# Performance work log

Measured on AMD Instinct MI355X. Metric: run time of the kernel, lower is better.

Reference implementation:

```python
import jax, jax.numpy as jnp
import numpy as np

HIDDEN = 1024
HEADS = 16
HEAD_DIM = HIDDEN // HEADS
B, S = 2, 2048


def setup_inputs() -> dict:
    key = jax.random.key(0)
    k1, k2, k3 = jax.random.split(key, 3)
    x = jax.random.normal(k1, (B, S, HIDDEN), dtype=jnp.float32)
    qkv_w = jax.random.normal(k2, (3 * HIDDEN, HIDDEN), dtype=jnp.float32) * (HIDDEN ** -0.5)
    out_w = jax.random.normal(k3, (HIDDEN, HIDDEN), dtype=jnp.float32) * (HIDDEN ** -0.5)
    return {"x": x, "qkv_w": qkv_w, "out_w": out_w}


def reference(x, qkv_w, out_w):
    b, s, d = x.shape
    scale = HEAD_DIM ** -0.5
    # qkv projection (Linear without bias: x @ W^T)
    qkv = x @ qkv_w.T                                   # [b, s, 3d]
    qkv = qkv.reshape(b, s, 3, HEADS, HEAD_DIM)
    qkv = jnp.transpose(qkv, (2, 0, 3, 1, 4))           # [3, b, h, s, hd]
    q, k, v = qkv[0] * scale, qkv[1], qkv[2]
    # causal attention (blocked torch loop == full causal softmax attention)
    scores = jnp.einsum('bhqd,bhkd->bhqk', q, k)        # [b, h, s, s]
    causal = jnp.tril(jnp.ones((s, s), dtype=bool))
    scores = jnp.where(causal[None, None], scores, -jnp.inf)
    weights = jax.nn.softmax(scores, axis=-1)
    attn = jnp.einsum('bhqk,bhkd->bhqd', weights, v)    # [b, h, s, hd]
    attn = jnp.transpose(attn, (0, 2, 1, 3)).reshape(b, s, d)
    return attn @ out_w.T
```

## Files before the change

### kernel.cpp

```cpp
#include <hip/hip_runtime.h>
#include <hip/hip_bf16.h>
#include <math.h>

#define HIDDEN 1024
#define HEADS 16
#define HDIM 64
#define BATCH 2
#define SEQ 2048
#define BHN (BATCH*HEADS)
#define MTOT (BATCH*SEQ)

typedef __attribute__((ext_vector_type(8))) short short8;
typedef __attribute__((ext_vector_type(4))) short short4v;
typedef __attribute__((ext_vector_type(4))) float floatx4;

#define GL2LDS(gsrc, ldst) __builtin_amdgcn_global_load_lds( \
    (const __attribute__((address_space(1))) void*)(gsrc), \
    (__attribute__((address_space(3))) void*)(ldst), 16, 0, 0)

__device__ __forceinline__ short f2bf(float f) {
  union { float f; unsigned u; } v; v.f = f;
  unsigned u = v.u;
  unsigned r = (u + 0x7fffu + ((u >> 16) & 1u)) >> 16;
  return (short)r;
}

__global__ __launch_bounds__(256) void cvt3_f32_bf16(
    const float* __restrict__ a, const float* __restrict__ b, const float* __restrict__ c,
    short* __restrict__ oa, short* __restrict__ ob, short* __restrict__ oc) {
  int i = blockIdx.x * 256 + threadIdx.x;
  const float* src; short* dst; int j;
  if (i < 1048576)      { src = a; dst = oa; j = i; }
  else if (i < 1835008) { src = b; dst = ob; j = i - 1048576; }
  else                  { src = c; dst = oc; j = i - 1835008; }
  float4 f = reinterpret_cast<const float4*>(src)[j];
  short4 o;
  o.x = f2bf(f.x); o.y = f2bf(f.y); o.z = f2bf(f.z); o.w = f2bf(f.w);
  reinterpret_cast<short4*>(dst)[j] = o;
}

template<int EPI, int BN>
__global__ __launch_bounds__(256) void gemm_bt(
    const short* __restrict__ A, const short* __restrict__ B,
    int M, int N, int K,
    float* __restrict__ outF,
    short* __restrict__ outQ, short* __restrict__ outK, short* __restrict__ outV)
{
  constexpr int WN = BN / 2;
  constexpr int NI = BN / 32;
  constexpr int BRD = BN / 32;
  __shared__ __align__(16) short As[128*64];
  __shared__ __align__(16) short Bs[BN*64];
  const int tid = threadIdx.x;
  const int wv = tid >> 6;
  const int lane = tid & 63;
  const int l15 = lane & 15;
  const int quad = lane >> 4;
  const int swl = l15 & 7;
  const int wm = wv >> 1, wn = wv & 1;

  const int nwg = gridDim.x * gridDim.y;
  const int cpx = nwg >> 3;
  int wg = (int)blockIdx.y * gridDim.x + blockIdx.x;
  wg = (wg & 7) * cpx + (wg >> 3);
  const int bx = wg % gridDim.x, by = wg / gridDim.x;
  const int row0 = by * 128, col0 = bx * BN;

  const int nsteps = K >> 6;

  const short* aSrc[4];
#pragma unroll
  for (int rd = 0; rd < 4; ++rd) {
    int chunk = rd * 256 + tid;
    int r = chunk >> 3, c = ((chunk & 7) ^ (r & 7)) << 3;
    aSrc[rd] = A + (long)(row0 + r) * K + c;
  }
  const short* bSrc[BRD];
#pragma unroll
  for (int rd = 0; rd < BRD; ++rd) {
    int chunk = rd * 256 + tid;
    int r = chunk >> 3, c = ((chunk & 7) ^ (r & 7)) << 3;
    bSrc[rd] = B + (long)(col0 + r) * K + c;
  }

  floatx4 acc[4][NI];
#pragma unroll
  for (int i = 0; i < 4; i++)
#pragma unroll
    for (int j = 0; j < NI; j++) acc[i][j] = (floatx4){0.f, 0.f, 0.f, 0.f};

  for (int t = 0; t < nsteps; ++t) {
#pragma unroll
    for (int rd = 0; rd < 4; ++rd) {
      GL2LDS(aSrc[rd], As + (rd * 256 + wv * 64) * 8);
      aSrc[rd] += 64;
    }
#pragma unroll
    for (int rd = 0; rd < BRD; ++rd) {
      GL2LDS(bSrc[rd], Bs + (rd * 256 + wv * 64) * 8);
      bSrc[rd] += 64;
    }
    __syncthreads();

    short8 af[4][2], bfr[NI][2];
#pragma unroll
    for (int mi = 0; mi < 4; mi++) {
      const short* ap = As + (wm * 64 + mi * 16 + l15) * 64;
#pragma unroll
      for (int kk = 0; kk < 2; kk++)
        af[mi][kk] = *(const short8*)(ap + (((kk * 4 + quad) ^ swl) << 3));
    }
#pragma unroll
    for (int ni = 0; ni < NI; ni++) {
      const short* bp = Bs + (wn * WN + ni * 16 + l15) * 64;
#pragma unroll
      for (int kk = 0; kk < 2; kk++)
        bfr[ni][kk] = *(const short8*)(bp + (((kk * 4 + quad) ^ swl) << 3));
    }
    __builtin_amdgcn_s_setprio(1);
#pragma unroll
    for (int mi = 0; mi < 4; mi++)
#pragma unroll
      for (int ni = 0; ni < NI; ni++)
#pragma unroll
        for (int kk = 0; kk < 2; kk++)
          acc[mi][ni] = __builtin_amdgcn_mfma_f32_16x16x32_bf16(af[mi][kk], bfr[ni][kk], acc[mi][ni], 0, 0, 0);
    __builtin_amdgcn_s_setprio(0);
    __syncthreads();
  }

  if (EPI == 2) {
#pragma unroll
    for (int mi = 0; mi < 4; mi++) {
      int rr = row0 + wm * 64 + mi * 16 + quad * 4;
#pragma unroll
      for (int ni = 0; ni < NI; ni++) {
        int cc = col0 + wn * WN + ni * 16 + l15;
#pragma unroll
        for (int r = 0; r < 4; r++)
          outF[(long)(rr + r) * N + cc] = acc[mi][ni][r];
      }
    }
  } else {
#pragma unroll
    for (int mi = 0; mi < 4; mi++) {
      int rowg = row0 + wm * 64 + mi * 16 + quad * 4;
#pragma unroll
      for (int ni = 0; ni < NI; ni++) {
        int j = col0 + wn * WN + ni * 16 + l15;
        int t = j >> 10;
        int rem = j & 1023;
        int h = rem >> 6, d = rem & 63;
#pragma unroll
        for (int r = 0; r < 4; r++) {
          int i = rowg + r;
          int b = i >> 11, s = i & 2047;
          int bh = b * HEADS + h;
          float v = acc[mi][ni][r];
          if (t == 0)      outQ[(bh * SEQ + s) * HDIM + d] = f2bf(v * 0.18033688011112042f);
          else if (t == 1) outK[(bh * SEQ + s) * HDIM + d] = f2bf(v);
          else             outV[(bh * HDIM + d) * SEQ + s] = f2bf(v);
        }
      }
    }
  }
}

__global__ __launch_bounds__(256, 4) void flash_attn(
    const short* __restrict__ qg, const short* __restrict__ kg,
    const short* __restrict__ vT, short* __restrict__ attn)
{
  __shared__ __align__(16) short Ks[2][64 * 64];
  __shared__ __align__(16) short Vs[2][64 * 64];

  const int tid = threadIdx.x;
  const int wv = tid >> 6, lane = tid & 63;
  const int l15 = lane & 15, quad = lane >> 4;
  const int bh = blockIdx.x;
  const int yl = (int)blockIdx.y;
  const int sgrp = yl >> 3, y0 = yl & 7;
  const int yp = ((sgrp >> 1) << 4) + ((sgrp & 1) ? (15 - y0) : y0);
  const int rt = 31 - yp;
  const int qh = wv >> 1;
  const int kh = wv & 1;
  const int m0 = rt * 64 + qh * 32;
  const int swl = l15 & 7;

  const short* kPtr[2];
  const short* vPtr[2];
  int ldsOff[2];
#pragma unroll
  for (int i = 0; i < 2; ++i) {
    int slot = i * 256 + tid;
    int r = slot >> 3;
    int c = ((slot & 7) ^ (r & 7)) << 3;
    kPtr[i] = kg + (bh * SEQ + r) * HDIM + c;
    vPtr[i] = vT + (bh * HDIM + r) * SEQ + c;
    ldsOff[i] = (i * 256 + wv * 64) * 8;
  }
#define STAGE_KV(KsB, VsB)                              \
  do {                                                  \
    _Pragma("unroll")                                   \
    for (int i = 0; i < 2; ++i) {                       \
      GL2LDS(kPtr[i], (KsB) + ldsOff[i]);               \
      GL2LDS(vPtr[i], (VsB) + ldsOff[i]);               \
      kPtr[i] += 64 * HDIM;                             \
      vPtr[i] += 64;                                    \
    }                                                   \
  } while (0)

  short8 aq[2][2];
#pragma unroll
  for (int g = 0; g < 2; g++) {
    const short* qp = qg + (long)(bh * SEQ + m0 + g * 16 + l15) * HDIM + quad * 8;
    aq[g][0] = *(const short8*)qp;
    aq[g][1] = *(const short8*)(qp + 32);
  }

  const short ONE = (short)0x3F80;
  const short4v ones4 = {ONE, ONE, ONE, ONE};

  floatx4 o[2][4], lsum[2];
#pragma unroll
  for (int g = 0; g < 2; g++) {
    lsum[g] = (floatx4){0.f, 0.f, 0.f, 0.f};
#pragma unroll
    for (int nt = 0; nt < 4; nt++) o[g][nt] = (floatx4){0.f, 0.f, 0.f, 0.f};
  }

  const int ntiles = rt + 1;
  STAGE_KV(Ks[0], Vs[0]);

  for (int kt = 0; kt < ntiles; ++kt) {
    __syncthreads();
    const int buf = kt & 1;
    if (kt + 1 < ntiles)
      STAGE_KV(Ks[buf ^ 1], Vs[buf ^ 1]);

    const short* KsB = Ks[buf];
    const short* VsB = Vs[buf];

    floatx4 sc[2][2];
#pragma unroll
    for (int g = 0; g < 2; g++)
#pragma unroll
      for (int sub = 0; sub < 2; sub++) sc[g][sub] = (floatx4){0.f, 0.f, 0.f, 0.f};
    __builtin_amdgcn_s_setprio(1);
#pragma unroll
    for (int sub = 0; sub < 2; sub++) {
      const short* kp = KsB + (kh * 32 + sub * 16 + l15) * 64;
      short8 kf0 = *(const short8*)(kp + ((quad ^ swl) << 3));
      short8 kf1 = *(const short8*)(kp + (((4 + quad) ^ swl) << 3));
#pragma unroll
      for (int g = 0; g < 2; g++) {
        sc[g][sub] = __builtin_amdgcn_mfma_f32_16x16x32_bf16(kf0, aq[g][0], sc[g][sub], 0, 0, 0);
        sc[g][sub] = __builtin_amdgcn_mfma_f32_16x16x32_bf16(kf1, aq[g][1], sc[g][sub], 0, 0, 0);
      }
    }
    __builtin_amdgcn_s_setprio(0);

    short4v pa[2][2];
#pragma unroll
    for (int g = 0; g < 2; g++) {
      const int qrow = m0 + g * 16 + l15;
#pragma unroll
      for (int sub = 0; sub < 2; sub++) {
        const int kbase = kt * 64 + kh * 32 + sub * 16;
        const bool full = (kbase + 15) <= (m0 + g * 16);
        unsigned u[4];
#pragma unroll
        for (int r = 0; r < 4; r++) {
          float pe = __builtin_amdgcn_exp2f(sc[g][sub][r]);
          if (!full) {
            const int kpos = kbase + quad * 4 + r;
            pe = (kpos <= qrow) ? pe : 0.f;
          }
          u[r] = __builtin_bit_cast(unsigned, pe);
        }
        uint2 w;
        w.x = __builtin_amdgcn_perm(u[1], u[0], 0x07060302);
        w.y = __builtin_amdgcn_perm(u[3], u[2], 0x07060302);
        pa[g][sub] = __builtin_bit_cast(short4v, w);
      }
    }

    __builtin_amdgcn_s_setprio(1);
#pragma unroll
    for (int sub = 0; sub < 2; sub++) {
      short4v bv[4];
#pragma unroll
      for (int nt = 0; nt < 4; nt++) {
        const int ch = (kh * 4 + sub * 2 + (quad >> 1)) ^ swl;
        bv[nt] = *(const short4v*)(VsB + (nt * 16 + l15) * 64 + (ch << 3) + ((quad & 1) << 2));
      }
#pragma unroll
      for (int g = 0; g < 2; g++) {
        lsum[g] = __builtin_amdgcn_mfma_f32_16x16x16bf16_1k(pa[g][sub], ones4, lsum[g], 0, 0, 0);
#pragma unroll
        for (int nt = 0; nt < 4; nt++)
          o[g][nt] = __builtin_amdgcn_mfma_f32_16x16x16bf16_1k(pa[g][sub], bv[nt], o[g][nt], 0, 0, 0);
      }
    }
    __builtin_amdgcn_s_setprio(0);
  }
#undef STAGE_KV

  __syncthreads();
  float* redO = (float*)&Ks[0][0];
  float* redL = (float*)&Vs[0][0];
  const int thr = qh * 64 + lane;
  if (kh == 1) {
#pragma unroll
    for (int g = 0; g < 2; g++) {
#pragma unroll
      for (int nt = 0; nt < 4; nt++)
#pragma unroll
        for (int r = 0; r < 4; r++)
          redO[(g * 16 + nt * 4 + r) * 128 + thr] = o[g][nt][r];
#pragma unroll
      for (int r = 0; r < 4; r++) redL[(g * 4 + r) * 128 + thr] = lsum[g][r];
    }
  }
  __syncthreads();
  if (kh == 0) {
    const int b = bh >> 4, h = bh & 15;
#pragma unroll
    for (int g = 0; g < 2; g++) {
      floatx4 lt = lsum[g];
#pragma unroll
      for (int r = 0; r < 4; r++) lt[r] += redL[(g * 4 + r) * 128 + thr];
#pragma unroll
      for (int r = 0; r < 4; r++) {
        const float inv = 1.0f / lt[r];
        const int srow = m0 + g * 16 + quad * 4 + r;
#pragma unroll
        for (int nt = 0; nt < 4; nt++) {
          float val = o[g][nt][r] + redO[(g * 16 + nt * 4 + r) * 128 + thr];
          attn[(long)(b * SEQ + srow) * HIDDEN + h * HDIM + nt * 16 + l15] = f2bf(val * inv);
        }
      }
    }
  }
}

extern "C" void kernel_launch(void* const* d_in, const int* in_sizes, int n_in,
                              void* d_out, int out_size, void* d_ws, size_t ws_size,
                              hipStream_t stream) {
  const float* x     = (const float*)d_in[0];
  const float* qkv_w = (const float*)d_in[1];
  const float* out_w = (const float*)d_in[2];
  float* out = (float*)d_out;

  short* xb   = (short*)d_ws;
  short* wqb  = xb  + MTOT * HIDDEN;
  short* wob  = wqb + 3 * HIDDEN * HIDDEN;
  short* qB   = wob + HIDDEN * HIDDEN;
  short* kB   = qB  + BHN * SEQ * HDIM;
  short* vTB  = kB  + BHN * SEQ * HDIM;
  short* attn = vTB + BHN * SEQ * HDIM;

  cvt3_f32_bf16<<<dim3(8192), dim3(256), 0, stream>>>(x, qkv_w, out_w, xb, wqb, wob);

  gemm_bt<1, 128><<<dim3(3 * HIDDEN / 128, MTOT / 128), dim3(256), 0, stream>>>(
      xb, wqb, MTOT, 3 * HIDDEN, HIDDEN, nullptr, qB, kB, vTB);

  flash_attn<<<dim3(BHN, SEQ / 64), dim3(256), 0, stream>>>(qB, kB, vTB, attn);

  gemm_bt<2, 64><<<dim3(HIDDEN / 64, MTOT / 128), dim3(256), 0, stream>>>(
      attn, wob, MTOT, HIDDEN, HIDDEN, out, nullptr, nullptr, nullptr);
}
```

Measured before the change: 171.4 us.

## Load K/V fragments directly from global memory, dropping LDS double-buffering

Removes the LDS staging of K and V tiles and the per-tile barrier. Each wave now loads its own K and V MFMA fragments straight from global memory into registers, and LDS is kept only for the final cross-wave reduction. This is meant to remove the barrier and LDS round-trip costs. In exchange, the two q-half waves sharing a kh slice read the same K/V data from global/L2 redundantly, and without prefetch the global load latency sits directly on the critical path.

After: 223.5 us. 30.5% more time.

```diff
diff --git a/kernel.cpp b/kernel.cpp
--- a/kernel.cpp
+++ b/kernel.cpp
@@ -170,8 +170,8 @@
     const short* __restrict__ qg, const short* __restrict__ kg,
     const short* __restrict__ vT, short* __restrict__ attn)
 {
-  __shared__ __align__(16) short Ks[2][64 * 64];
-  __shared__ __align__(16) short Vs[2][64 * 64];
+  __shared__ float redO[32 * 128];
+  __shared__ float redL[8 * 128];
 
   const int tid = threadIdx.x;
   const int wv = tid >> 6, lane = tid & 63;
@@ -184,30 +184,6 @@
   const int qh = wv >> 1;
   const int kh = wv & 1;
   const int m0 = rt * 64 + qh * 32;
-  const int swl = l15 & 7;
-
-  const short* kPtr[2];
-  const short* vPtr[2];
-  int ldsOff[2];
-#pragma unroll
-  for (int i = 0; i < 2; ++i) {
-    int slot = i * 256 + tid;
-    int r = slot >> 3;
-    int c = ((slot & 7) ^ (r & 7)) << 3;
-    kPtr[i] = kg + (bh * SEQ + r) * HDIM + c;
-    vPtr[i] = vT + (bh * HDIM + r) * SEQ + c;
-    ldsOff[i] = (i * 256 + wv * 64) * 8;
-  }
-#define STAGE_KV(KsB, VsB)                              \
-  do {                                                  \
-    _Pragma("unroll")                                   \
-    for (int i = 0; i < 2; ++i) {                       \
-      GL2LDS(kPtr[i], (KsB) + ldsOff[i]);               \
-      GL2LDS(vPtr[i], (VsB) + ldsOff[i]);               \
-      kPtr[i] += 64 * HDIM;                             \
-      vPtr[i] += 64;                                    \
-    }                                                   \
-  } while (0)
 
   short8 aq[2][2];
 #pragma unroll
@@ -217,6 +193,15 @@
     aq[g][1] = *(const short8*)(qp + 32);
   }
 
+  const short* kp[2];
+#pragma unroll
+  for (int sub = 0; sub < 2; sub++)
+    kp[sub] = kg + ((long)bh * SEQ + kh * 32 + sub * 16 + l15) * HDIM + quad * 8;
+  const short* vp[4];
+#pragma unroll
+  for (int nt = 0; nt < 4; nt++)
+    vp[nt] = vT + ((long)bh * HDIM + nt * 16 + l15) * SEQ + kh * 32 + quad * 4;
+
   const short ONE = (short)0x3F80;
   const short4v ones4 = {ONE, ONE, ONE, ONE};
 
@@ -229,16 +214,23 @@
   }
 
   const int ntiles = rt + 1;
-  STAGE_KV(Ks[0], Vs[0]);
 
   for (int kt = 0; kt < ntiles; ++kt) {
-    __syncthreads();
-    const int buf = kt & 1;
-    if (kt + 1 < ntiles)
-      STAGE_KV(Ks[buf ^ 1], Vs[buf ^ 1]);
-
-    const short* KsB = Ks[buf];
-    const short* VsB = Vs[buf];
+    short8 kf[2][2];
+#pragma unroll
+    for (int sub = 0; sub < 2; sub++) {
+      kf[sub][0] = *(const short8*)(kp[sub]);
+      kf[sub][1] = *(const short8*)(kp[sub] + 32);
+      kp[sub] += 64 * HDIM;
+    }
+    short4v bv[2][4];
+#pragma unroll
+    for (int nt = 0; nt < 4; nt++) {
+#pragma unroll
+      for (int sub = 0; sub < 2; sub++)
+        bv[sub][nt] = *(const short4v*)(vp[nt] + sub * 16);
+      vp[nt] += 64;
+    }
 
     floatx4 sc[2][2];
 #pragma unroll
@@ -247,16 +239,12 @@
       for (int sub = 0; sub < 2; sub++) sc[g][sub] = (floatx4){0.f, 0.f, 0.f, 0.f};
     __builtin_amdgcn_s_setprio(1);
 #pragma unroll
-    for (int sub = 0; sub < 2; sub++) {
-      const short* kp = KsB + (kh * 32 + sub * 16 + l15) * 64;
-      short8 kf0 = *(const short8*)(kp + ((quad ^ swl) << 3));
-      short8 kf1 = *(const short8*)(kp + (((4 + quad) ^ swl) << 3));
+    for (int sub = 0; sub < 2; sub++)
 #pragma unroll
       for (int g = 0; g < 2; g++) {
-        sc[g][sub] = __builtin_amdgcn_mfma_f32_16x16x32_bf16(kf0, aq[g][0], sc[g][sub], 0, 0, 0);
-        sc[g][sub] = __builtin_amdgcn_mfma_f32_16x16x32_bf16(kf1, aq[g][1], sc[g][sub], 0, 0, 0);
-      }
-    }
+        sc[g][sub] = __builtin_amdgcn_mfma_f32_16x16x32_bf16(kf[sub][0], aq[g][0], sc[g][sub], 0, 0, 0);
+        sc[g][sub] = __builtin_amdgcn_mfma_f32_16x16x32_bf16(kf[sub][1], aq[g][1], sc[g][sub], 0, 0, 0);
+      }
     __builtin_amdgcn_s_setprio(0);
 
     short4v pa[2][2];
@@ -286,28 +274,18 @@
 
     __builtin_amdgcn_s_setprio(1);
 #pragma unroll
-    for (int sub = 0; sub < 2; sub++) {
-      short4v bv[4];
-#pragma unroll
-      for (int nt = 0; nt < 4; nt++) {
-        const int ch = (kh * 4 + sub * 2 + (quad >> 1)) ^ swl;
-        bv[nt] = *(const short4v*)(VsB + (nt * 16 + l15) * 64 + (ch << 3) + ((quad & 1) << 2));
-      }
+    for (int sub = 0; sub < 2; sub++)
 #pragma unroll
       for (int g = 0; g < 2; g++) {
         lsum[g] = __builtin_amdgcn_mfma_f32_16x16x16bf16_1k(pa[g][sub], ones4, lsum[g], 0, 0, 0);
 #pragma unroll
         for (int nt = 0; nt < 4; nt++)
-          o[g][nt] = __builtin_amdgcn_mfma_f32_16x16x16bf16_1k(pa[g][sub], bv[nt], o[g][nt], 0, 0, 0);
-      }
-    }
+          o[g][nt] = __builtin_amdgcn_mfma_f32_16x16x16bf16_1k(pa[g][sub], bv[sub][nt], o[g][nt], 0, 0, 0);
+      }
     __builtin_amdgcn_s_setprio(0);
   }
-#undef STAGE_KV
 
   __syncthreads();
-  float* redO = (float*)&Ks[0][0];
-  float* redL = (float*)&Vs[0][0];
   const int thr = qh * 64 + lane;
   if (kh == 1) {
 #pragma unroll
```
